# Performance work log

Hardware: AMD Instinct MI355X
Metric: run time of the kernel (lower is better)

## Reference

```python
import jax, jax.numpy as jnp
import numpy as np
from jax import lax

B, T, D, H = 2048, 512, 88, 16


def setup_inputs() -> dict:
    key = jax.random.key(0)
    k1, k2, k3, k4 = jax.random.split(key, 4)
    # binary piano-roll observations [num_sequences, max_length, data_dim]
    sequences = (jax.random.uniform(k1, (B, T, D)) < 0.5).astype(jnp.float32)
    # simplex transition matrix [H, H]
    probs_x = jax.nn.softmax(jax.random.normal(k2, (H, H)), axis=-1)
    # unit-interval emission probs [H, D]
    probs_y = jax.nn.sigmoid(jax.random.normal(k3, (H, D)))
    lengths = jax.random.randint(k4, (B,), 1, T + 1).astype(jnp.int32)
    mb = jnp.arange(B, dtype=jnp.int64)
    mask = jnp.ones((B,), dtype=bool)
    scale = jnp.float32(1.0)
    return {"sequences": sequences, "probs_x": probs_x, "probs_y": probs_y,
            "scale": scale, "lengths": lengths, "mb": mb, "mask": mask}


def reference(sequences, probs_x, probs_y, scale, lengths, mb, mask):
    # Minibatch selection (mb indexes sequences/lengths, as in the pyro model)
    seq = sequences[mb]            # [B, T, D]
    lens = lengths[mb]             # [B]
    log_A = jnp.log(probs_x)       # [H, H] transition log-probs
    log_py = jnp.log(probs_y)      # [H, D]
    log_1mpy = jnp.log1p(-probs_y)
    # Bernoulli emission log-likelihood summed over tones plate: [B, T, H]
    emit = (jnp.einsum('btd,hd->bth', seq, log_py)
            + jnp.einsum('btd,hd->bth', 1.0 - seq, log_1mpy))
    NEG = jnp.float32(-1e30)
    # x starts at state 0 before the first transition -> delta at state 0
    alpha0 = jnp.full((seq.shape[0], log_A.shape[0]), NEG).at[:, 0].set(0.0)

    def step(alpha, inp):
        emit_t, t = inp            # emit_t: [B, H]
        nxt = jax.nn.logsumexp(alpha[:, :, None] + log_A[None], axis=1) + emit_t
        valid = (t < lens)[:, None]  # handlers.mask(t < lengths)
        return jnp.where(valid, nxt, alpha), None

    emit_tbh = jnp.swapaxes(emit, 0, 1)          # [T, B, H]
    alphaT, _ = lax.scan(step, alpha0, (emit_tbh, jnp.arange(emit_tbh.shape[0])))
    ll = jax.nn.logsumexp(alphaT, axis=-1)       # marginal log-lik per sequence
    # sequences-plate mask + handlers.scale
    return scale * jnp.where(mask, ll, 0.0)
```

## Files before the change

### kernel.cpp

```cpp
#include <hip/hip_runtime.h>

#define B_N 2048
#define T_N 512
#define D_N 88
#define H_N 16
#define NEGF (-1e30f)
#define LN2F 0.69314718055994530942f

typedef __attribute__((ext_vector_type(8))) short short8;
typedef __attribute__((ext_vector_type(4))) float floatx4;

template<int CTRL>
__device__ __forceinline__ float dppf(float x) {
    return __int_as_float(__builtin_amdgcn_update_dpp(
        0, __float_as_int(x), CTRL, 0xF, 0xF, false));
}

__device__ __forceinline__ float grp16_max(float v) {
    v = fmaxf(v, dppf<0x128>(v));
    v = fmaxf(v, dppf<0x124>(v));
    v = fmaxf(v, dppf<0x122>(v));
    v = fmaxf(v, dppf<0x121>(v));
    return v;
}
__device__ __forceinline__ float grp16_sum(float v) {
    v += dppf<0x128>(v);
    v += dppf<0x124>(v);
    v += dppf<0x122>(v);
    v += dppf<0x121>(v);
    return v;
}

__device__ __forceinline__ ushort bf16rne(float f) {
    unsigned u = __float_as_uint(f);
    u += 0x7FFFu + ((u >> 16) & 1u);
    return (ushort)(u >> 16);
}

__device__ __forceinline__ void calib(const float* __restrict__ px, int h,
                                      float (&aro)[16]) {
    float idxf = (float)h;
    aro[0]  = px[h * 16 + h];
    aro[1]  = px[((int)dppf<0x121>(idxf)) * 16 + h];
    aro[2]  = px[((int)dppf<0x122>(idxf)) * 16 + h];
    aro[3]  = px[((int)dppf<0x123>(idxf)) * 16 + h];
    aro[4]  = px[((int)dppf<0x124>(idxf)) * 16 + h];
    aro[5]  = px[((int)dppf<0x125>(idxf)) * 16 + h];
    aro[6]  = px[((int)dppf<0x126>(idxf)) * 16 + h];
    aro[7]  = px[((int)dppf<0x127>(idxf)) * 16 + h];
    aro[8]  = px[((int)dppf<0x128>(idxf)) * 16 + h];
    aro[9]  = px[((int)dppf<0x129>(idxf)) * 16 + h];
    aro[10] = px[((int)dppf<0x12A>(idxf)) * 16 + h];
    aro[11] = px[((int)dppf<0x12B>(idxf)) * 16 + h];
    aro[12] = px[((int)dppf<0x12C>(idxf)) * 16 + h];
    aro[13] = px[((int)dppf<0x12D>(idxf)) * 16 + h];
    aro[14] = px[((int)dppf<0x12E>(idxf)) * 16 + h];
    aro[15] = px[((int)dppf<0x12F>(idxf)) * 16 + h];
}

__device__ __forceinline__ float matvec16(float p, const float (&aro)[16]) {
    float a0 = p * aro[0];
    float a1 = dppf<0x121>(p) * aro[1];
    float a2 = dppf<0x122>(p) * aro[2];
    float a3 = dppf<0x123>(p) * aro[3];
    a0 += dppf<0x124>(p) * aro[4];
    a1 += dppf<0x125>(p) * aro[5];
    a2 += dppf<0x126>(p) * aro[6];
    a3 += dppf<0x127>(p) * aro[7];
    a0 += dppf<0x128>(p) * aro[8];
    a1 += dppf<0x129>(p) * aro[9];
    a2 += dppf<0x12A>(p) * aro[10];
    a3 += dppf<0x12B>(p) * aro[11];
    a0 += dppf<0x12C>(p) * aro[12];
    a1 += dppf<0x12D>(p) * aro[13];
    a2 += dppf<0x12E>(p) * aro[14];
    a3 += dppf<0x12F>(p) * aro[15];
    return (a0 + a1) + (a2 + a3);
}

__device__ __forceinline__ void hmm_step(float& aRel, float& M, float emit2,
                                         bool valid, const float (&aro)[16]) {
    float p = exp2f(aRel);
    float s = matvec16(p, aro);
    float g = __log2f(s) + emit2;
    float mg = grp16_max(g);
    if (valid) { aRel = g - mg; M = M + mg; }
}

__global__ void hmm_prep(const float* __restrict__ probs_y,
                         ushort* __restrict__ bpack, float* __restrict__ base) {
    int tid = threadIdx.x;
    for (int i = tid; i < 3 * 64 * 8; i += 256) {
        int k = i >> 9;
        int l = (i >> 3) & 63;
        int j = i & 7;
        int kk = k * 32 + ((l >> 4) * 8) + j;
        int h = l & 15;
        ushort v = 0;
        if (kk < D_N) {
            float p = probs_y[h * D_N + kk];
            v = bf16rne(log2f(p) - log2f(1.0f - p));
        }
        bpack[i] = v;
    }
    if (tid < H_N) {
        float s = 0.0f;
        for (int d = 0; d < D_N; ++d)
            s += log2f(1.0f - probs_y[tid * D_N + d]);
        base[tid] = s;
    }
}

__global__ __launch_bounds__(256) void hmm_emit(
    const float* __restrict__ seq, const int* __restrict__ lengths,
    const ushort* __restrict__ bpack, const float* __restrict__ base,
    ushort* __restrict__ wBuf, float* __restrict__ cBuf) {
    int bid = blockIdx.x;
    int b = bid >> 3;
    int t0 = (bid & 7) * 64;
    if (t0 >= lengths[b]) return;

    __shared__ ushort sA[64 * 104];
    int tid = threadIdx.x;
    const float* gseq = seq + ((size_t)b * T_N + t0) * D_N;

    for (int f = tid; f < 768; f += 256) {
        if (f < 704) {
            int r = f / 11;
            int c = f - r * 11;
            const float* gp = gseq + f * 8;
            float4 v0 = *(const float4*)(gp);
            float4 v1 = *(const float4*)(gp + 4);
            uint4 w;
            w.x = (__float_as_uint(v0.x) >> 16) | (__float_as_uint(v0.y) & 0xFFFF0000u);
            w.y = (__float_as_uint(v0.z) >> 16) | (__float_as_uint(v0.w) & 0xFFFF0000u);
            w.z = (__float_as_uint(v1.x) >> 16) | (__float_as_uint(v1.y) & 0xFFFF0000u);
            w.w = (__float_as_uint(v1.z) >> 16) | (__float_as_uint(v1.w) & 0xFFFF0000u);
            *(uint4*)(&sA[r * 104 + c * 8]) = w;
        } else {
            int r = f - 704;
            uint4 z; z.x = 0; z.y = 0; z.z = 0; z.w = 0;
            *(uint4*)(&sA[r * 104 + 88]) = z;
        }
    }
    __syncthreads();

    int l = tid & 63, w = tid >> 6;
    int q = l >> 4, h = l & 15;

    const short8* bp = (const short8*)bpack;
    short8 bf0 = bp[l];
    short8 bf1 = bp[64 + l];
    short8 bf2 = bp[128 + l];

    int arow = w * 16 + h;
    short8 af0 = *(const short8*)&sA[arow * 104 + 0  + q * 8];
    short8 af1 = *(const short8*)&sA[arow * 104 + 32 + q * 8];
    short8 af2 = *(const short8*)&sA[arow * 104 + 64 + q * 8];

    floatx4 acc = {0.f, 0.f, 0.f, 0.f};
    acc = __builtin_amdgcn_mfma_f32_16x16x32_bf16(af0, bf0, acc, 0, 0, 0);
    acc = __builtin_amdgcn_mfma_f32_16x16x32_bf16(af1, bf1, acc, 0, 0, 0);
    acc = __builtin_amdgcn_mfma_f32_16x16x32_bf16(af2, bf2, acc, 0, 0, 0);

    float bh = base[h];
    float e0 = acc[0] + bh, e1 = acc[1] + bh, e2 = acc[2] + bh, e3 = acc[3] + bh;
    float c0 = grp16_max(e0), c1 = grp16_max(e1);
    float c2 = grp16_max(e2), c3 = grp16_max(e3);

    int tloc = t0 + w * 16 + q * 4;
    ushort4 wv;
    wv.x = bf16rne(exp2f(e0 - c0));
    wv.y = bf16rne(exp2f(e1 - c1));
    wv.z = bf16rne(exp2f(e2 - c2));
    wv.w = bf16rne(exp2f(e3 - c3));
    *(ushort4*)&wBuf[((size_t)(b * H_N + h)) * T_N + tloc] = wv;
    if (h == 0) {
        float4 cv; cv.x = c0; cv.y = c1; cv.z = c2; cv.w = c3;
        *(float4*)&cBuf[(size_t)b * T_N + tloc] = cv;
    }
}

__global__ __launch_bounds__(64) void hmm_scan(
    const float* __restrict__ probs_x, const ushort* __restrict__ wBuf,
    const float* __restrict__ cBuf, const int* __restrict__ lengths,
    const float* __restrict__ scale, float* __restrict__ out) {
    int lane = threadIdx.x;
    int sl = lane >> 4, h = lane & 15;
    int b0 = blockIdx.x * 4;
    int b = b0 + sl;
    int len = lengths[b];

    float aro[16];
    calib(probs_x, h, aro);

    int wmax = max(max(lengths[b0], lengths[b0 + 1]),
                   max(lengths[b0 + 2], lengths[b0 + 3]));

    const ushort4* eb = (const ushort4*)(wBuf + ((size_t)(b * H_N + h)) * T_N);
    const float4*  cb = (const float4*)(cBuf + (size_t)b * T_N);
    float aLin = (h == 0) ? 1.0f : 0.0f;
    float M = 0.0f;

    int nch = (wmax + 3) >> 2;
    ushort4 wA = eb[0], wB = eb[1], wC = eb[2];
    float4  cA = cb[0], cB = cb[1], cC = cb[2];
    for (int c = 0; c < nch; ++c) {
        ushort4 wD = eb[c + 3];
        float4  cD = cb[c + 3];
        float f0 = __uint_as_float((unsigned)wA.x << 16);
        float f1 = __uint_as_float((unsigned)wA.y << 16);
        float f2 = __uint_as_float((unsigned)wA.z << 16);
        float f3 = __uint_as_float((unsigned)wA.w << 16);
        int t0c = c * 4;
        float s;
        s = matvec16(aLin, aro); if (t0c + 0 < len) { aLin = s * f0; M += cA.x; }
        s = matvec16(aLin, aro); if (t0c + 1 < len) { aLin = s * f1; M += cA.y; }
        s = matvec16(aLin, aro); if (t0c + 2 < len) { aLin = s * f2; M += cA.z; }
        s = matvec16(aLin, aro); if (t0c + 3 < len) { aLin = s * f3; M += cA.w; }
        float mx = grp16_max(aLin);
        unsigned ex = (__float_as_uint(mx) >> 23) & 0xFFu;
        aLin *= __uint_as_float((254u - ex) << 23);
        M += (float)((int)ex - 127);
        wA = wB; wB = wC; wC = wD;
        cA = cB; cB = cC; cC = cD;
    }
    float ssum = grp16_sum(aLin);
    if (h == 0)
        out[b] = scale[0] * (LN2F * (M + __log2f(ssum)));
}

__global__ __launch_bounds__(64) void hmm_fused_naive(
    const float* __restrict__ seq, const float* __restrict__ px,
    const float* __restrict__ py, const float* __restrict__ sc,
    const int* __restrict__ lengths, float* __restrict__ out) {
    int lane = threadIdx.x;
    int sl = lane >> 4, h = lane & 15;
    int b0 = blockIdx.x * 4;
    int b = b0 + sl;
    int len = lengths[b];

    float aro[16];
    calib(px, h, aro);

    float wreg[88];
    float b2 = 0.0f;
#pragma unroll
    for (int d = 0; d < D_N; ++d) {
        float p = py[h * D_N + d];
        float l1 = log2f(1.0f - p);
        wreg[d] = log2f(p) - l1;
        b2 += l1;
    }
    int wmax = max(max(lengths[b0], lengths[b0 + 1]),
                   max(lengths[b0 + 2], lengths[b0 + 3]));

    float aRel = (h == 0) ? 0.0f : NEGF;
    float M = 0.0f;
    for (int t = 0; t < wmax; ++t) {
        const float4* sp = (const float4*)(seq + ((size_t)b * T_N + t) * D_N);
        float e = b2;
#pragma unroll
        for (int j = 0; j < 22; ++j) {
            float4 v = sp[j];
            e += v.x * wreg[4 * j] + v.y * wreg[4 * j + 1] +
                 v.z * wreg[4 * j + 2] + v.w * wreg[4 * j + 3];
        }
        hmm_step(aRel, M, e, t < len, aro);
    }
    float pf = exp2f(aRel);
    float s = grp16_sum(pf);
    if (h == 0)
        out[b] = sc[0] * (LN2F * (M + __log2f(s)));
}

extern "C" void kernel_launch(void* const* d_in, const int* in_sizes, int n_in,
                              void* d_out, int out_size, void* d_ws,
                              size_t ws_size, hipStream_t stream) {
    const float* seq = (const float*)d_in[0];
    const float* px  = (const float*)d_in[1];
    const float* py  = (const float*)d_in[2];
    const float* sc  = (const float*)d_in[3];
    const int*   len = (const int*)d_in[4];
    float* out = (float*)d_out;

    size_t w_elems = (size_t)B_N * H_N * T_N;
    size_t c_elems = (size_t)B_N * T_N;
    size_t need = w_elems * 2 + c_elems * 4 + 16 * 4 + 1536 * 2 + 256;
    if (ws_size >= need) {
        ushort* wBuf  = (ushort*)d_ws;
        float*  cBuf  = (float*)(wBuf + w_elems);
        float*  base  = cBuf + c_elems;
        ushort* bpack = (ushort*)(base + 16);
        hmm_prep<<<1, 256, 0, stream>>>(py, bpack, base);
        hmm_emit<<<B_N * 8, 256, 0, stream>>>(seq, len, bpack, base, wBuf, cBuf);
        hmm_scan<<<B_N / 4, 64, 0, stream>>>(px, wBuf, cBuf, len, sc, out);
    } else {
        hmm_fused_naive<<<B_N / 4, 64, 0, stream>>>(seq, px, py, sc, len, out);
    }
}
```

Baseline: 528.8 us.

## Run HMM forward scan as batched MFMA over 16 sequences per wave

After: 522.2 us. Within noise of the previous version (-1.2%).

```diff
diff --git a/kernel.cpp b/kernel.cpp
--- a/kernel.cpp
+++ b/kernel.cpp
@@ -8,6 +8,7 @@
 #define LN2F 0.69314718055994530942f
 
 typedef __attribute__((ext_vector_type(8))) short short8;
+typedef __attribute__((ext_vector_type(4))) short short4v;
 typedef __attribute__((ext_vector_type(4))) float floatx4;
 
 template<int CTRL>
@@ -35,6 +36,28 @@
     unsigned u = __float_as_uint(f);
     u += 0x7FFFu + ((u >> 16) & 1u);
     return (ushort)(u >> 16);
+}
+
+__device__ __forceinline__ unsigned packbf(float x, float y) {
+    return (__float_as_uint(x) >> 16) | (__float_as_uint(y) & 0xFFFF0000u);
+}
+
+__device__ __forceinline__ float swz_xor16_f(float v) {
+    return __int_as_float(
+        __builtin_amdgcn_ds_swizzle(__float_as_int(v), 0x401F));
+}
+
+__device__ __forceinline__ floatx4 mfma16(short4v a, short4v b) {
+    floatx4 z = {0.f, 0.f, 0.f, 0.f};
+#if __has_builtin(__builtin_amdgcn_mfma_f32_16x16x16bf16_1k)
+    return __builtin_amdgcn_mfma_f32_16x16x16bf16_1k(a, b, z, 0, 0, 0);
+#else
+    floatx4 d;
+    asm volatile("v_mfma_f32_16x16x16_bf16 %0, %1, %2, %3\n\t"
+                 "s_nop 7\n\ts_nop 7"
+                 : "=&v"(d) : "v"(a), "v"(b), "v"(z));
+    return d;
+#endif
 }
 
 __device__ __forceinline__ void calib(const float* __restrict__ px, int h,
@@ -88,7 +111,8 @@
 }
 
 __global__ void hmm_prep(const float* __restrict__ probs_y,
-                         ushort* __restrict__ bpack, float* __restrict__ base) {
+                         ushort* __restrict__ bpack, float* __restrict__ base,
+                         float* __restrict__ cSum) {
     int tid = threadIdx.x;
     for (int i = tid; i < 3 * 64 * 8; i += 256) {
         int k = i >> 9;
@@ -103,6 +127,7 @@
         }
         bpack[i] = v;
     }
+    for (int i = tid; i < B_N; i += 256) cSum[i] = 0.0f;
     if (tid < H_N) {
         float s = 0.0f;
         for (int d = 0; d < D_N; ++d)
@@ -114,11 +139,13 @@
 __global__ __launch_bounds__(256) void hmm_emit(
     const float* __restrict__ seq, const int* __restrict__ lengths,
     const ushort* __restrict__ bpack, const float* __restrict__ base,
-    ushort* __restrict__ wBuf, float* __restrict__ cBuf) {
+    ushort* __restrict__ wBuf, float* __restrict__ cSum) {
     int bid = blockIdx.x;
     int b = bid >> 3;
     int t0 = (bid & 7) * 64;
-    if (t0 >= lengths[b]) return;
+    int len = lengths[b];
+    if (t0 >= len) return;
+    int lenLoc = min(len - t0, 64);
 
     __shared__ ushort sA[64 * 104];
     int tid = threadIdx.x;
@@ -127,16 +154,18 @@
     for (int f = tid; f < 768; f += 256) {
         if (f < 704) {
             int r = f / 11;
-            int c = f - r * 11;
-            const float* gp = gseq + f * 8;
-            float4 v0 = *(const float4*)(gp);
-            float4 v1 = *(const float4*)(gp + 4);
-            uint4 w;
-            w.x = (__float_as_uint(v0.x) >> 16) | (__float_as_uint(v0.y) & 0xFFFF0000u);
-            w.y = (__float_as_uint(v0.z) >> 16) | (__float_as_uint(v0.w) & 0xFFFF0000u);
-            w.z = (__float_as_uint(v1.x) >> 16) | (__float_as_uint(v1.y) & 0xFFFF0000u);
-            w.w = (__float_as_uint(v1.z) >> 16) | (__float_as_uint(v1.w) & 0xFFFF0000u);
-            *(uint4*)(&sA[r * 104 + c * 8]) = w;
+            if (r < lenLoc) {
+                int c = f - r * 11;
+                const float* gp = gseq + f * 8;
+                float4 v0 = *(const float4*)(gp);
+                float4 v1 = *(const float4*)(gp + 4);
+                uint4 w;
+                w.x = (__float_as_uint(v0.x) >> 16) | (__float_as_uint(v0.y) & 0xFFFF0000u);
+                w.y = (__float_as_uint(v0.z) >> 16) | (__float_as_uint(v0.w) & 0xFFFF0000u);
+                w.z = (__float_as_uint(v1.x) >> 16) | (__float_as_uint(v1.y) & 0xFFFF0000u);
+                w.w = (__float_as_uint(v1.z) >> 16) | (__float_as_uint(v1.w) & 0xFFFF0000u);
+                *(uint4*)(&sA[r * 104 + c * 8]) = w;
+            }
         } else {
             int r = f - 704;
             uint4 z; z.x = 0; z.y = 0; z.z = 0; z.w = 0;
@@ -168,66 +197,96 @@
     float c0 = grp16_max(e0), c1 = grp16_max(e1);
     float c2 = grp16_max(e2), c3 = grp16_max(e3);
 
-    int tloc = t0 + w * 16 + q * 4;
-    ushort4 wv;
-    wv.x = bf16rne(exp2f(e0 - c0));
-    wv.y = bf16rne(exp2f(e1 - c1));
-    wv.z = bf16rne(exp2f(e2 - c2));
-    wv.w = bf16rne(exp2f(e3 - c3));
-    *(ushort4*)&wBuf[((size_t)(b * H_N + h)) * T_N + tloc] = wv;
-    if (h == 0) {
-        float4 cv; cv.x = c0; cv.y = c1; cv.z = c2; cv.w = c3;
-        *(float4*)&cBuf[(size_t)b * T_N + tloc] = cv;
-    }
-}
-
-__global__ __launch_bounds__(64) void hmm_scan(
-    const float* __restrict__ probs_x, const ushort* __restrict__ wBuf,
-    const float* __restrict__ cBuf, const int* __restrict__ lengths,
+    int tRow = t0 + w * 16 + q * 4;
+    size_t wb = ((size_t)b * T_N + tRow) * H_N + h;
+    wBuf[wb]      = bf16rne(exp2f(e0 - c0));
+    wBuf[wb + 16] = bf16rne(exp2f(e1 - c1));
+    wBuf[wb + 32] = bf16rne(exp2f(e2 - c2));
+    wBuf[wb + 48] = bf16rne(exp2f(e3 - c3));
+
+    float cs = 0.0f;
+    if (tRow + 0 < len) cs += c0;
+    if (tRow + 1 < len) cs += c1;
+    if (tRow + 2 < len) cs += c2;
+    if (tRow + 3 < len) cs += c3;
+    cs += swz_xor16_f(cs);
+    cs += __shfl_xor(cs, 32, 64);
+    if (l == 0) atomicAdd(&cSum[b], cs);
+}
+
+__global__ __launch_bounds__(64) void hmm_scan_mfma(
+    const float* __restrict__ px, const ushort* __restrict__ wBuf,
+    const float* __restrict__ cSum, const int* __restrict__ lengths,
     const float* __restrict__ scale, float* __restrict__ out) {
     int lane = threadIdx.x;
-    int sl = lane >> 4, h = lane & 15;
-    int b0 = blockIdx.x * 4;
-    int b = b0 + sl;
+    int s = lane & 15, q = lane >> 4;
+    int b0 = blockIdx.x * 16;
+    int b = b0 + s;
     int len = lengths[b];
-
-    float aro[16];
-    calib(probs_x, h, aro);
-
-    int wmax = max(max(lengths[b0], lengths[b0 + 1]),
-                   max(lengths[b0 + 2], lengths[b0 + 3]));
-
-    const ushort4* eb = (const ushort4*)(wBuf + ((size_t)(b * H_N + h)) * T_N);
-    const float4*  cb = (const float4*)(cBuf + (size_t)b * T_N);
-    float aLin = (h == 0) ? 1.0f : 0.0f;
-    float M = 0.0f;
-
-    int nch = (wmax + 3) >> 2;
-    ushort4 wA = eb[0], wB = eb[1], wC = eb[2];
-    float4  cA = cb[0], cB = cb[1], cC = cb[2];
-    for (int c = 0; c < nch; ++c) {
-        ushort4 wD = eb[c + 3];
-        float4  cD = cb[c + 3];
-        float f0 = __uint_as_float((unsigned)wA.x << 16);
-        float f1 = __uint_as_float((unsigned)wA.y << 16);
-        float f2 = __uint_as_float((unsigned)wA.z << 16);
-        float f3 = __uint_as_float((unsigned)wA.w << 16);
-        int t0c = c * 4;
-        float s;
-        s = matvec16(aLin, aro); if (t0c + 0 < len) { aLin = s * f0; M += cA.x; }
-        s = matvec16(aLin, aro); if (t0c + 1 < len) { aLin = s * f1; M += cA.y; }
-        s = matvec16(aLin, aro); if (t0c + 2 < len) { aLin = s * f2; M += cA.z; }
-        s = matvec16(aLin, aro); if (t0c + 3 < len) { aLin = s * f3; M += cA.w; }
-        float mx = grp16_max(aLin);
-        unsigned ex = (__float_as_uint(mx) >> 23) & 0xFFu;
-        aLin *= __uint_as_float((254u - ex) << 23);
-        M += (float)((int)ex - 127);
-        wA = wB; wB = wC; wC = wD;
-        cA = cB; cB = cC; cC = cD;
-    }
-    float ssum = grp16_sum(aLin);
-    if (h == 0)
-        out[b] = scale[0] * (LN2F * (M + __log2f(ssum)));
+    int wmax = (int)__builtin_amdgcn_readfirstlane(grp16_max((float)len));
+
+    short4v af;
+#pragma unroll
+    for (int j = 0; j < 4; ++j)
+        af[j] = (short)bf16rne(px[(q * 4 + j) * 16 + (lane & 15)]);
+
+    float a0 = (q == 0) ? 1.0f : 0.0f, a1 = 0.f, a2 = 0.f, a3 = 0.f;
+    unsigned bp0 = packbf(a0, a1), bp1 = packbf(a2, a3);
+
+    float fin = 0.f, finM = 0.f, M = 0.f;
+    float S = 1.0f, Epend = 0.0f;
+
+    const ushort4* wp = (const ushort4*)wBuf;
+    size_t idx0 = (size_t)b * (T_N * 4) + q;
+
+    ushort4 rA[8], rB[8];
+#pragma unroll
+    for (int j = 0; j < 8; ++j) rA[j] = wp[idx0 + (size_t)j * 4];
+
+    int ngrp = (wmax + 7) >> 3;
+    for (int g = 0; g < ngrp; ++g) {
+        int tg = g * 8;
+#pragma unroll
+        for (int j = 0; j < 8; ++j)
+            rB[j] = wp[idx0 + (size_t)(tg + 8 + j) * 4];
+#pragma unroll
+        for (int j = 0; j < 8; ++j) {
+            ushort4 w4 = rA[j];
+            float w0 = __uint_as_float((unsigned)w4.x << 16);
+            float w1 = __uint_as_float((unsigned)w4.y << 16);
+            float w2 = __uint_as_float((unsigned)w4.z << 16);
+            float w3 = __uint_as_float((unsigned)w4.w << 16);
+            if (j == 1) {
+                w0 *= S; w1 *= S; w2 *= S; w3 *= S;
+                M += Epend;
+            }
+            union { unsigned u[2]; short4v v; } bu;
+            bu.u[0] = bp0; bu.u[1] = bp1;
+            floatx4 d = mfma16(af, bu.v);
+            a0 = d[0] * w0; a1 = d[1] * w1; a2 = d[2] * w2; a3 = d[3] * w3;
+            bp0 = packbf(a0, a1); bp1 = packbf(a2, a3);
+            int t = tg + j;
+            bool snap = (t == len - 1);
+            float s4 = (a0 + a1) + (a2 + a3);
+            fin  = snap ? s4 : fin;
+            finM = snap ? M : finM;
+            if (j == 7) {
+                float mx = fmaxf(fmaxf(a0, a1), fmaxf(a2, a3));
+                mx = fmaxf(mx, swz_xor16_f(mx));
+                mx = fmaxf(mx, __shfl_xor(mx, 32, 64));
+                unsigned ex = (__float_as_uint(mx) >> 23) & 0xFFu;
+                S = __uint_as_float((254u - ex) << 23);
+                Epend = (float)((int)ex - 127);
+            }
+        }
+#pragma unroll
+        for (int j = 0; j < 8; ++j) rA[j] = rB[j];
+    }
+    float tot = fin;
+    tot += swz_xor16_f(tot);
+    tot += __shfl_xor(tot, 32, 64);
+    float ll = LN2F * (cSum[b] + finM + __log2f(tot));
+    if (lane < 16) out[b] = scale[0] * ll;
 }
 
 __global__ __launch_bounds__(64) void hmm_fused_naive(
@@ -285,16 +344,15 @@
     float* out = (float*)d_out;
 
     size_t w_elems = (size_t)B_N * H_N * T_N;
-    size_t c_elems = (size_t)B_N * T_N;
-    size_t need = w_elems * 2 + c_elems * 4 + 16 * 4 + 1536 * 2 + 256;
+    size_t need = w_elems * 2 + B_N * 4 + 16 * 4 + 1536 * 2 + 4096;
     if (ws_size >= need) {
         ushort* wBuf  = (ushort*)d_ws;
-        float*  cBuf  = (float*)(wBuf + w_elems);
-        float*  base  = cBuf + c_elems;
+        float*  cSum  = (float*)(wBuf + w_elems);
+        float*  base  = cSum + B_N;
         ushort* bpack = (ushort*)(base + 16);
-        hmm_prep<<<1, 256, 0, stream>>>(py, bpack, base);
-        hmm_emit<<<B_N * 8, 256, 0, stream>>>(seq, len, bpack, base, wBuf, cBuf);
-        hmm_scan<<<B_N / 4, 64, 0, stream>>>(px, wBuf, cBuf, len, sc, out);
+        hmm_prep<<<1, 256, 0, stream>>>(py, bpack, base, cSum);
+        hmm_emit<<<B_N * 8, 256, 0, stream>>>(seq, len, bpack, base, wBuf, cSum);
+        hmm_scan_mfma<<<B_N / 16, 64, 0, stream>>>(px, wBuf, cSum, len, sc, out);
     } else {
         hmm_fused_naive<<<B_N / 4, 64, 0, stream>>>(seq, px, py, sc, len, out);
     }
```
